# Kernel tuning notes

Hardware: AMD Instinct MI355X
Metric: run time of the kernel (lower is better)

Reference implementation:

```python
import jax, jax.numpy as jnp
import numpy as np

H_DIM = 1024
NHEADS = 16
HEAD = H_DIM // NHEADS


def setup_inputs() -> dict:
    key = jax.random.key(0)
    ks = jax.random.split(key, 7)
    B, T = 2, 2048
    s = 1.0 / np.sqrt(H_DIM)
    return {
        "x": jax.random.normal(ks[0], (B, T, H_DIM), dtype=jnp.float32),
        "Wq": jax.random.uniform(ks[1], (H_DIM, H_DIM), jnp.float32, -s, s),
        "bq": jax.random.uniform(ks[2], (H_DIM,), jnp.float32, -s, s),
        "Wk": jax.random.uniform(ks[3], (H_DIM, H_DIM), jnp.float32, -s, s),
        "bk": jax.random.uniform(ks[4], (H_DIM,), jnp.float32, -s, s),
        "Wv": jax.random.uniform(ks[5], (H_DIM, H_DIM), jnp.float32, -s, s),
        "bv": jax.random.uniform(ks[6], (H_DIM,), jnp.float32, -s, s),
    }


def _split_heads(a, B, T):
    # [B, T, h_dim] -> [B, nH, T, head]
    return a.reshape(B, T, NHEADS, HEAD).transpose(0, 2, 1, 3)


def reference(x, Wq, bq, Wk, bk, Wv, bv):
    B, T, allH = x.shape
    q = _split_heads(x @ Wq.T + bq, B, T)
    k = _split_heads(x @ Wk.T + bk, B, T)
    v = _split_heads(x @ Wv.T + bv, B, T)
    # NOTE: original scales by sqrt(h_dim) (full hidden), not sqrt(head_dim)
    att = jnp.einsum("bhqd,bhkd->bhqk", q, k) / jnp.sqrt(jnp.float32(allH))
    causal = jnp.tril(jnp.ones((T, T), dtype=bool))
    att = jnp.where(causal, att, -jnp.inf)
    att = jax.nn.softmax(att, axis=-1)
    out = jnp.einsum("bhqk,bhkd->bhqd", att, v)
    return out.transpose(0, 2, 1, 3).reshape(B, T, allH)
```

## Files before the change

### kernel.cpp

```cpp
#include <hip/hip_runtime.h>
#include <math.h>

typedef __bf16 bf16;
typedef __bf16 bf16x8 __attribute__((ext_vector_type(8)));
typedef __bf16 bf16x4 __attribute__((ext_vector_type(4)));
typedef __bf16 bf16x2 __attribute__((ext_vector_type(2)));
typedef float floatx4 __attribute__((ext_vector_type(4)));
typedef float floatx16 __attribute__((ext_vector_type(16)));
typedef unsigned int uintx4 __attribute__((ext_vector_type(4)));

#define T_SEQ 2048
#define NH 16
#define HD 64
#define HDIM 1024
#define BATCH 2
#define SCALE 0.03125f

static __device__ __forceinline__ floatx4 mfma16(bf16x8 a, bf16x8 b, floatx4 c) {
  return __builtin_amdgcn_mfma_f32_16x16x32_bf16(a, b, c, 0, 0, 0);
}
static __device__ __forceinline__ floatx16 mfma32(bf16x8 a, bf16x8 b, floatx16 c) {
  return __builtin_amdgcn_mfma_f32_32x32x16_bf16(a, b, c, 0, 0, 0);
}

static __device__ __forceinline__ unsigned int packbf(float a, float b) {
  bf16x2 t; t[0] = (bf16)a; t[1] = (bf16)b;
  return __builtin_bit_cast(unsigned int, t);
}

static __device__ __forceinline__ bf16x8 cvt_pack(floatx4 lo, floatx4 hi) {
  bf16x8 r;
  r[0] = (bf16)lo[0]; r[1] = (bf16)lo[1]; r[2] = (bf16)lo[2]; r[3] = (bf16)lo[3];
  r[4] = (bf16)hi[0]; r[5] = (bf16)hi[1]; r[6] = (bf16)hi[2]; r[7] = (bf16)hi[3];
  return r;
}

typedef const __attribute__((address_space(1))) void* gas_ptr;
typedef __attribute__((address_space(3))) void* las_ptr;
static __device__ __forceinline__ void load_lds16(const bf16* g, bf16* l) {
  __builtin_amdgcn_global_load_lds((gas_ptr)g, (las_ptr)l, 16, 0, 0);
}

__global__ __launch_bounds__(256) void cvt_f32_bf16(
    const float* __restrict__ x, const float* __restrict__ Wq,
    const float* __restrict__ Wk, const float* __restrict__ Wv,
    bf16* __restrict__ xb, bf16* __restrict__ wb) {
  const int seg = blockIdx.y;
  const float* src; bf16* dst; int n;
  if (seg == 0)      { src = x;  dst = xb;                 n = BATCH * T_SEQ * HDIM; }
  else if (seg == 1) { src = Wq; dst = wb;                 n = HDIM * HDIM; }
  else if (seg == 2) { src = Wk; dst = wb + HDIM * HDIM;   n = HDIM * HDIM; }
  else               { src = Wv; dst = wb + 2*HDIM*HDIM;   n = HDIM * HDIM; }
  const int i4 = (blockIdx.x * 256 + threadIdx.x) * 4;
  if (i4 < n) {
    floatx4 v = *(const floatx4*)(src + i4);
    bf16x4 o; o[0]=(bf16)v[0]; o[1]=(bf16)v[1]; o[2]=(bf16)v[2]; o[3]=(bf16)v[3];
    *(bf16x4*)(dst + i4) = o;
  }
}

__global__ __launch_bounds__(256) void qkv_gemm_lds(
    const bf16* __restrict__ xb, const bf16* __restrict__ wb,
    const float* __restrict__ bq, const float* __restrict__ bk,
    const float* __restrict__ bv, bf16* __restrict__ qkv) {
  __shared__ __align__(16) bf16 smem[16384];

  const int m0  = blockIdx.x * 128;
  const int n0g = blockIdx.y * 128;
  const int z   = n0g >> 10;
  const float* bias = (z == 0) ? bq : (z == 1) ? bk : bv;
  bf16* out = qkv + (size_t)z * BATCH * T_SEQ * HDIM;

  const int lane = threadIdx.x & 63;
  const int w    = threadIdx.x >> 6;
  const int l15  = lane & 15;
  const int quad = lane >> 4;
  const int wm = w & 1, wn = w >> 1;

  const int srow = w * 32 + (lane >> 2);
  const int scol = (lane & 3) * 8;
  const bf16* aG0 = xb + (size_t)(m0 + srow) * HDIM + scol;
  const bf16* aG1 = xb + (size_t)(m0 + srow + 16) * HDIM + scol;
  const bf16* bG0 = wb + (size_t)(n0g + srow) * HDIM + scol;
  const bf16* bG1 = wb + (size_t)(n0g + srow + 16) * HDIM + scol;

#define GSTAGE(BUF, KOFF)                                                    \
  {                                                                          \
    bf16* aB = smem + (BUF) * 4096;                                          \
    bf16* bB = smem + 8192 + (BUF) * 4096;                                   \
    load_lds16(aG0 + (KOFF), aB + (w * 32) * 32);                            \
    load_lds16(aG1 + (KOFF), aB + (w * 32 + 16) * 32);                       \
    load_lds16(bG0 + (KOFF), bB + (w * 32) * 32);                            \
    load_lds16(bG1 + (KOFF), bB + (w * 32 + 16) * 32);                       \
  }

  floatx4 acc[4][4] = {};

  GSTAGE(0, 0);
  __syncthreads();

  for (int k0 = 0; k0 < 32; ++k0) {
    const int cur = k0 & 1;
    if (k0 < 31) GSTAGE(cur ^ 1, (k0 + 1) * 32);

    const bf16* A = smem + cur * 4096;
    const bf16* B = smem + 8192 + cur * 4096;

    bf16x8 af[4], bf[4];
#pragma unroll
    for (int i = 0; i < 4; ++i)
      af[i] = *(const bf16x8*)(A + (wm * 64 + i * 16 + l15) * 32 + quad * 8);
#pragma unroll
    for (int jj = 0; jj < 4; ++jj)
      bf[jj] = *(const bf16x8*)(B + (wn * 64 + jj * 16 + l15) * 32 + quad * 8);
#pragma unroll
    for (int i = 0; i < 4; ++i)
#pragma unroll
      for (int jj = 0; jj < 4; ++jj)
        acc[i][jj] = mfma16(af[i], bf[jj], acc[i][jj]);

    __syncthreads();
  }
#undef GSTAGE

  const size_t bhS = (size_t)T_SEQ * HD;
  for (int jj = 0; jj < 4; ++jj) {
    const int nloc = (n0g + wn * 64 + jj * 16 + l15) & (HDIM - 1);
    const float bvv = bias[nloc];
    const int h = nloc >> 6, d = nloc & (HD - 1);
    for (int i = 0; i < 4; ++i) {
      for (int r = 0; r < 4; ++r) {
        const int gm = m0 + wm * 64 + i * 16 + quad * 4 + r;
        const int bb = gm >> 11, t = gm & (T_SEQ - 1);
        const bf16 val = (bf16)(acc[i][jj][r] + bvv);
        bf16* obh = out + (size_t)(bb * NH + h) * bhS;
        if (z == 0) {
          obh[(size_t)t * HD + d] = val;
        } else if (z == 1) {
          obh[(t >> 5) * 2048 + (d >> 4) * 512 +
              ((t & 31) + ((d >> 3) & 1) * 32) * 8 + (d & 7)] = val;
        } else {
          obh[(t >> 5) * 2048 + (((t >> 4) & 1) + ((d >> 5) << 1)) * 512 +
              ((d & 31) + ((t >> 3) & 1) * 32) * 8 + (t & 7)] = val;
        }
      }
    }
  }
}

#define LSTR 40

__global__ __launch_bounds__(256) void qkv_gemm_f32(
    const float* __restrict__ x,
    const float* __restrict__ Wq, const float* __restrict__ bq,
    const float* __restrict__ Wk, const float* __restrict__ bk,
    const float* __restrict__ Wv, const float* __restrict__ bv,
    bf16* __restrict__ qkv) {
  __shared__ __align__(16) bf16 As[128 * LSTR];
  __shared__ __align__(16) bf16 Bs[128 * LSTR];

  const int n0g = blockIdx.y * 128;
  const int z   = n0g >> 10;
  const int n0  = n0g & (HDIM - 1);
  const float* W    = (z == 0) ? Wq : (z == 1) ? Wk : Wv;
  const float* bias = (z == 0) ? bq : (z == 1) ? bk : bv;
  bf16* out = qkv + (size_t)z * BATCH * T_SEQ * HDIM;
  const int m0 = blockIdx.x * 128;

  const int lane = threadIdx.x & 63;
  const int w    = threadIdx.x >> 6;
  const int l15  = lane & 15;
  const int quad = lane >> 4;
  const int wm = w & 1, wn = w >> 1;

  const int srow  = threadIdx.x >> 1;
  const int shalf = threadIdx.x & 1;
  const float* aSrc = x + (size_t)(m0 + srow) * HDIM + shalf * 16;
  const float* bSrc = W + (size_t)(n0 + srow) * HDIM + shalf * 16;
  bf16* aDst = As + srow * LSTR + shalf * 16;
  bf16* bDst = Bs + srow * LSTR + shalf * 16;

  floatx4 acc[4][4] = {};

  for (int k0 = 0; k0 < HDIM; k0 += 32) {
    floatx4 a0 = *(const floatx4*)(aSrc + k0);
    floatx4 a1 = *(const floatx4*)(aSrc + k0 + 4);
    floatx4 a2 = *(const floatx4*)(aSrc + k0 + 8);
    floatx4 a3 = *(const floatx4*)(aSrc + k0 + 12);
    floatx4 b0 = *(const floatx4*)(bSrc + k0);
    floatx4 b1 = *(const floatx4*)(bSrc + k0 + 4);
    floatx4 b2 = *(const floatx4*)(bSrc + k0 + 8);
    floatx4 b3 = *(const floatx4*)(bSrc + k0 + 12);

    __syncthreads();
    *(bf16x8*)(aDst)     = cvt_pack(a0, a1);
    *(bf16x8*)(aDst + 8) = cvt_pack(a2, a3);
    *(bf16x8*)(bDst)     = cvt_pack(b0, b1);
    *(bf16x8*)(bDst + 8) = cvt_pack(b2, b3);
    __syncthreads();

    bf16x8 af[4], bff[4];
    for (int i = 0; i < 4; ++i)
      af[i] = *(const bf16x8*)(As + (wm * 64 + i * 16 + l15) * LSTR + quad * 8);
    for (int jj = 0; jj < 4; ++jj)
      bff[jj] = *(const bf16x8*)(Bs + (wn * 64 + jj * 16 + l15) * LSTR + quad * 8);
    for (int i = 0; i < 4; ++i)
      for (int jj = 0; jj < 4; ++jj)
        acc[i][jj] = mfma16(af[i], bff[jj], acc[i][jj]);
  }

  for (int jj = 0; jj < 4; ++jj) {
    const int nloc = n0 + wn * 64 + jj * 16 + l15;
    const float bvv = bias[nloc];
    const int h = nloc >> 6, d = nloc & (HD - 1);
    for (int i = 0; i < 4; ++i) {
      for (int r = 0; r < 4; ++r) {
        const int gm = m0 + wm * 64 + i * 16 + quad * 4 + r;
        const int bb = gm >> 11, t = gm & (T_SEQ - 1);
        out[((size_t)((bb * NH + h) * T_SEQ) + t) * HD + d] = (bf16)(acc[i][jj][r] + bvv);
      }
    }
  }
}

#define ASTEP(G, QF, O0, O1, LL, DIAG)                                         \
  {                                                                            \
    const bf16* kp_ = Kb + (G) * 2048 + lane * 8;                              \
    bf16x8 kf0 = *(const bf16x8*)(kp_);                                        \
    bf16x8 kf1 = *(const bf16x8*)(kp_ + 512);                                  \
    bf16x8 kf2 = *(const bf16x8*)(kp_ + 1024);                                 \
    bf16x8 kf3 = *(const bf16x8*)(kp_ + 1536);                                 \
    const bf16* vp_ = Vb + (G) * 2048 + lane * 8;                              \
    bf16x8 v00 = *(const bf16x8*)(vp_);                                        \
    bf16x8 v01 = *(const bf16x8*)(vp_ + 512);                                  \
    bf16x8 v10 = *(const bf16x8*)(vp_ + 1024);                                 \
    bf16x8 v11 = *(const bf16x8*)(vp_ + 1536);                                 \
    floatx16 s = {};                                                           \
    s = mfma32(kf0, QF[0], s);                                                 \
    s = mfma32(kf1, QF[1], s);                                                 \
    s = mfma32(kf2, QF[2], s);                                                 \
    s = mfma32(kf3, QF[3], s);                                                 \
    float pp[16];                                                              \
    _Pragma("unroll")                                                          \
    for (int r = 0; r < 16; ++r) pp[r] = __expf(s[r]);                         \
    if (DIAG) {                                                                \
      _Pragma("unroll")                                                        \
      for (int r = 0; r < 16; ++r) {                                           \
        const int krow = (r & 3) + 8 * (r >> 2) + 4 * hf;                      \
        if (krow > l31) pp[r] = 0.f;                                           \
      }                                                                        \
    }                                                                          \
    float psum = 0.f;                                                          \
    _Pragma("unroll")                                                          \
    for (int r = 0; r < 16; ++r) psum += pp[r];                                \
    LL += psum;                                                                \
    unsigned int Dg[4][2], Xg[4][2];                                           \
    _Pragma("unroll")                                                          \
    for (int a = 0; a < 4; ++a) {                                              \
      Dg[a][0] = packbf(pp[4 * a + 0], pp[4 * a + 1]);                         \
      Dg[a][1] = packbf(pp[4 * a + 2], pp[4 * a + 3]);                         \
    }                                                                          \
    _Pragma("unroll")                                                          \
    for (int a = 0; a < 4; ++a) {                                              \
      Xg[a][0] = (unsigned int)__shfl_xor((int)Dg[a][0], 32, 64);              \
      Xg[a][1] = (unsigned int)__shfl_xor((int)Dg[a][1], 32, 64);              \
    }                                                                          \
    uintx4 f0u, f1u;                                                           \
    f0u[0] = hf ? Xg[1][0] : Dg[0][0];                                         \
    f0u[1] = hf ? Xg[1][1] : Dg[0][1];                                         \
    f0u[2] = hf ? Dg[1][0] : Xg[0][0];                                         \
    f0u[3] = hf ? Dg[1][1] : Xg[0][1];                                         \
    f1u[0] = hf ? Xg[3][0] : Dg[2][0];                                         \
    f1u[1] = hf ? Xg[3][1] : Dg[2][1];                                         \
    f1u[2] = hf ? Dg[3][0] : Xg[2][0];                                         \
    f1u[3] = hf ? Dg[3][1] : Xg[2][1];                                         \
    bf16x8 pf0 = __builtin_bit_cast(bf16x8, f0u);                              \
    bf16x8 pf1 = __builtin_bit_cast(bf16x8, f1u);                              \
    O0 = mfma32(v00, pf0, O0);                                                 \
    O0 = mfma32(v01, pf1, O0);                                                 \
    O1 = mfma32(v10, pf0, O1);                                                 \
    O1 = mfma32(v11, pf1, O1);                                                 \
  }

__global__ __launch_bounds__(256, 4) void attn_v13(
    const bf16* __restrict__ qkv, float* __restrict__ out) {
  const bf16* Q = qkv;

  __shared__ float ps[4][64][33];

  const int lane = threadIdx.x & 63;
  const int w    = threadIdx.x >> 6;
  const int l31  = lane & 31;
  const int hf   = lane >> 5;

  const int lin = blockIdx.x + (blockIdx.y << 5);
  const int bh  = ((lin & 7) << 2) + ((lin >> 3) & 3);
  const int pi  = lin >> 5;

  const int qtA = pi, qtB = 63 - pi;
  const int q0A = qtA * 32, q0B = qtB * 32;
  const int SA = qtA + 1;

  const bf16* Qb = Q + (size_t)bh * T_SEQ * HD;
  const bf16* Kb = qkv + (size_t)BATCH * T_SEQ * HDIM + (size_t)bh * T_SEQ * HD;
  const bf16* Vb = qkv + (size_t)2 * BATCH * T_SEQ * HDIM + (size_t)bh * T_SEQ * HD;
  const int b = bh >> 4, hh = bh & (NH - 1);

  bf16x8 qfA[4];
#pragma unroll
  for (int kk = 0; kk < 4; ++kk) {
    qfA[kk] = *(const bf16x8*)(Qb + (size_t)(q0A + l31) * HD + kk * 16 + hf * 8);
#pragma unroll
    for (int e = 0; e < 8; ++e) qfA[kk][e] = (bf16)((float)qfA[kk][e] * SCALE);
  }

  floatx16 oA0 = {}, oA1 = {};
  float laccA = 0.f;

  int g = w;
  for (; g < SA; g += 4)
    ASTEP(g, qfA, oA0, oA1, laccA, g == SA - 1);

  laccA += __shfl_xor(laccA, 32, 64);

#pragma unroll
  for (int r = 0; r < 16; ++r) {
    ps[w][lane][r]      = oA0[r];
    ps[w][lane][16 + r] = oA1[r];
  }
  ps[w][lane][32] = laccA;
  __syncthreads();
  {
    const float ls = ps[0][lane][32] + ps[1][lane][32] +
                     ps[2][lane][32] + ps[3][lane][32];
    const float inv = 1.f / ls;
    float* obA = out + ((size_t)(b * T_SEQ + q0A + l31)) * HDIM + hh * HD;
#pragma unroll
    for (int i = 0; i < 8; ++i) {
      const int rr = 8 * w + i;
      const float sv = ps[0][lane][rr] + ps[1][lane][rr] +
                       ps[2][lane][rr] + ps[3][lane][rr];
      const int r = rr & 15;
      const int drow = (r & 3) + 8 * (r >> 2) + 4 * hf + ((rr >= 16) ? 32 : 0);
      obA[drow] = sv * inv;
    }
  }
  __syncthreads();

  bf16x8 qfB[4];
#pragma unroll
  for (int kk = 0; kk < 4; ++kk) {
    qfB[kk] = *(const bf16x8*)(Qb + (size_t)(q0B + l31) * HD + kk * 16 + hf * 8);
#pragma unroll
    for (int e = 0; e < 8; ++e) qfB[kk][e] = (bf16)((float)qfB[kk][e] * SCALE);
  }

  floatx16 oB0 = {}, oB1 = {};
  float laccB = 0.f;

  for (; g < 65; g += 4)
    ASTEP(g - SA, qfB, oB0, oB1, laccB, g == 64);

  laccB += __shfl_xor(laccB, 32, 64);

#pragma unroll
  for (int r = 0; r < 16; ++r) {
    ps[w][lane][r]      = oB0[r];
    ps[w][lane][16 + r] = oB1[r];
  }
  ps[w][lane][32] = laccB;
  __syncthreads();
  {
    const float ls = ps[0][lane][32] + ps[1][lane][32] +
                     ps[2][lane][32] + ps[3][lane][32];
    const float inv = 1.f / ls;
    float* obB = out + ((size_t)(b * T_SEQ + q0B + l31)) * HDIM + hh * HD;
#pragma unroll
    for (int i = 0; i < 8; ++i) {
      const int rr = 8 * w + i;
      const float sv = ps[0][lane][rr] + ps[1][lane][rr] +
                       ps[2][lane][rr] + ps[3][lane][rr];
      const int r = rr & 15;
      const int drow = (r & 3) + 8 * (r >> 2) + 4 * hf + ((rr >= 16) ? 32 : 0);
      obB[drow] = sv * inv;
    }
  }
}

#define PSTR 40

__global__ __launch_bounds__(256) void attn_v4(
    const bf16* __restrict__ qkv, float* __restrict__ out) {
  const bf16* Q = qkv;
  const bf16* K = qkv + (size_t)BATCH * T_SEQ * HDIM;
  const bf16* V = K + (size_t)BATCH * T_SEQ * HDIM;

  __shared__ __align__(16) bf16 pl[4 * 16 * PSTR];

  const int lane = threadIdx.x & 63;
  const int w    = threadIdx.x >> 6;
  const int l15  = lane & 15;
  const int quad = lane >> 4;

  const int bh = blockIdx.x;
  const int j  = blockIdx.y;
  const bf16* Qb = Q + (size_t)bh * T_SEQ * HD;
  const bf16* Kb = K + (size_t)bh * T_SEQ * HD;
  const bf16* Vb = V + (size_t)bh * T_SEQ * HD;
  const int b = bh >> 4, h = bh & (NH - 1);

  const int qt = (w == 0) ? j : (w == 1) ? (63 - j) : (w == 2) ? (64 + j) : (127 - j);
  const int q0 = qt * 16;

  bf16* pw = pl + w * 16 * PSTR;

  bf16x8 qf0 = *(const bf16x8*)(Qb + (size_t)(q0 + l15) * HD + quad * 8);
  bf16x8 qf1 = *(const bf16x8*)(Qb + (size_t)(q0 + l15) * HD + 32 + quad * 8);
  for (int e = 0; e < 8; ++e) {
    qf0[e] = (bf16)((float)qf0[e] * SCALE);
    qf1[e] = (bf16)((float)qf1[e] * SCALE);
  }

  floatx4 o[4] = {};
  float lacc[4] = {0.f, 0.f, 0.f, 0.f};

  const int S = (qt >> 1) + 1;

  for (int s0 = 0; s0 < S; ++s0) {
    const int kv = s0 * 32;

    bf16 ve[4][8];
    for (int jjj = 0; jjj < 8; ++jjj) {
      const bf16* vrow = Vb + (size_t)(kv + quad * 8 + jjj) * HD + l15;
      for (int dt = 0; dt < 4; ++dt) ve[dt][jjj] = vrow[dt * 16];
    }

    floatx4 sa[2];
    for (int nt = 0; nt < 2; ++nt) {
      const int kbase = kv + nt * 16;
      bf16x8 k0 = *(const bf16x8*)(Kb + (size_t)(kbase + l15) * HD + quad * 8);
      bf16x8 k1 = *(const bf16x8*)(Kb + (size_t)(kbase + l15) * HD + 32 + quad * 8);
      floatx4 s = {};
      s = mfma16(qf0, k0, s);
      s = mfma16(qf1, k1, s);
      sa[nt] = s;
    }

    float p[2][4];
    for (int nt = 0; nt < 2; ++nt)
      for (int r = 0; r < 4; ++r) p[nt][r] = __expf(sa[nt][r]);
    if (s0 == S - 1) {
      for (int nt = 0; nt < 2; ++nt) {
        const int kg = kv + nt * 16 + l15;
        for (int r = 0; r < 4; ++r) {
          const int qg = q0 + quad * 4 + r;
          if (kg > qg) p[nt][r] = 0.f;
        }
      }
    }
    for (int r = 0; r < 4; ++r) lacc[r] += p[0][r] + p[1][r];

    for (int nt = 0; nt < 2; ++nt)
      for (int r = 0; r < 4; ++r)
        pw[(quad * 4 + r) * PSTR + nt * 16 + l15] = (bf16)p[nt][r];
    __asm__ __volatile__("s_waitcnt lgkmcnt(0)" ::: "memory");
    const bf16x8 pf = *(const bf16x8*)(pw + l15 * PSTR + quad * 8);

    for (int dt = 0; dt < 4; ++dt) {
      bf16x8 vf;
      for (int jjj = 0; jjj < 8; ++jjj) vf[jjj] = ve[dt][jjj];
      o[dt] = mfma16(pf, vf, o[dt]);
    }
  }

  for (int r = 0; r < 4; ++r) {
    float v = lacc[r];
    for (int off = 1; off < 16; off <<= 1) v += __shfl_xor(v, off, 64);
    lacc[r] = v;
  }

  for (int dt = 0; dt < 4; ++dt) {
    for (int r = 0; r < 4; ++r) {
      const int t = q0 + quad * 4 + r;
      out[((size_t)(b * T_SEQ + t) * HDIM) + h * HD + dt * 16 + l15] =
          o[dt][r] / lacc[r];
    }
  }
}

extern "C" void kernel_launch(void* const* d_in, const int* in_sizes, int n_in,
                              void* d_out, int out_size, void* d_ws, size_t ws_size,
                              hipStream_t stream) {
  const float* x  = (const float*)d_in[0];
  const float* Wq = (const float*)d_in[1];
  const float* bq = (const float*)d_in[2];
  const float* Wk = (const float*)d_in[3];
  const float* bk = (const float*)d_in[4];
  const float* Wv = (const float*)d_in[5];
  const float* bv = (const float*)d_in[6];
  float* out = (float*)d_out;

  const size_t elems = (size_t)BATCH * T_SEQ * HDIM;
  bf16* qkv  = (bf16*)d_ws;
  bf16* xbuf = qkv + 3 * elems;
  bf16* wbuf = xbuf + elems;

  const bool fast = ws_size >= (size_t)39 * 1024 * 1024;
  dim3 g1(BATCH * T_SEQ / 128, 3 * HDIM / 128);
  if (fast) {
    cvt_f32_bf16<<<dim3(4096, 4), 256, 0, stream>>>(x, Wq, Wk, Wv, xbuf, wbuf);
    qkv_gemm_lds<<<g1, 256, 0, stream>>>(xbuf, wbuf, bq, bk, bv, qkv);
    attn_v13<<<dim3(BATCH * NH, 32), 256, 0, stream>>>(qkv, out);
  } else {
    qkv_gemm_f32<<<g1, 256, 0, stream>>>(x, Wq, bq, Wk, bk, Wv, bv, qkv);
    attn_v4<<<dim3(BATCH * NH, 32), 256, 0, stream>>>(qkv, out);
  }
}
```

Measured before the change: 151.5 us.

## Process two query tiles per K/V load in attention kernel

```diff
diff --git a/kernel.cpp b/kernel.cpp
--- a/kernel.cpp
+++ b/kernel.cpp
@@ -223,18 +223,8 @@
   }
 }
 
-#define ASTEP(G, QF, O0, O1, LL, DIAG)                                         \
+#define TBODY(QF, DIAG, O0, O1, LL)                                            \
   {                                                                            \
-    const bf16* kp_ = Kb + (G) * 2048 + lane * 8;                              \
-    bf16x8 kf0 = *(const bf16x8*)(kp_);                                        \
-    bf16x8 kf1 = *(const bf16x8*)(kp_ + 512);                                  \
-    bf16x8 kf2 = *(const bf16x8*)(kp_ + 1024);                                 \
-    bf16x8 kf3 = *(const bf16x8*)(kp_ + 1536);                                 \
-    const bf16* vp_ = Vb + (G) * 2048 + lane * 8;                              \
-    bf16x8 v00 = *(const bf16x8*)(vp_);                                        \
-    bf16x8 v01 = *(const bf16x8*)(vp_ + 512);                                  \
-    bf16x8 v10 = *(const bf16x8*)(vp_ + 1024);                                 \
-    bf16x8 v11 = *(const bf16x8*)(vp_ + 1536);                                 \
     floatx16 s = {};                                                           \
     s = mfma32(kf0, QF[0], s);                                                 \
     s = mfma32(kf1, QF[1], s);                                                 \
@@ -282,10 +272,49 @@
     O1 = mfma32(v11, pf1, O1);                                                 \
   }
 
-__global__ __launch_bounds__(256, 4) void attn_v13(
+#define ASTEP2(G, T0, QF0a, QF1a)                                              \
+  {                                                                            \
+    const int g_ = (G);                                                        \
+    const bf16* kp_ = Kb + g_ * 2048 + lane * 8;                               \
+    bf16x8 kf0 = *(const bf16x8*)(kp_);                                        \
+    bf16x8 kf1 = *(const bf16x8*)(kp_ + 512);                                  \
+    bf16x8 kf2 = *(const bf16x8*)(kp_ + 1024);                                 \
+    bf16x8 kf3 = *(const bf16x8*)(kp_ + 1536);                                 \
+    const bf16* vp_ = Vb + g_ * 2048 + lane * 8;                               \
+    bf16x8 v00 = *(const bf16x8*)(vp_);                                        \
+    bf16x8 v01 = *(const bf16x8*)(vp_ + 512);                                  \
+    bf16x8 v10 = *(const bf16x8*)(vp_ + 1024);                                 \
+    bf16x8 v11 = *(const bf16x8*)(vp_ + 1536);                                 \
+    if (g_ <= (T0)) TBODY(QF0a, g_ == (T0), o00, o01, l0);                     \
+    TBODY(QF1a, g_ == (T0) + 1, o10, o11, l1);                                 \
+  }
+
+#define COMBINE(O0, O1, LL, QROW)                                              \
+  {                                                                            \
+    _Pragma("unroll")                                                          \
+    for (int r = 0; r < 16; ++r) {                                             \
+      ps[w][lane][r]      = O0[r];                                             \
+      ps[w][lane][16 + r] = O1[r];                                             \
+    }                                                                          \
+    ps[w][lane][32] = LL;                                                      \
+    __syncthreads();                                                           \
+    const float ls = ps[0][lane][32] + ps[1][lane][32] +                       \
+                     ps[2][lane][32] + ps[3][lane][32];                        \
+    const float inv = 1.f / ls;                                                \
+    float* ob = out + ((size_t)(b * T_SEQ + (QROW))) * HDIM + hh * HD;         \
+    _Pragma("unroll")                                                          \
+    for (int i = 0; i < 8; ++i) {                                              \
+      const int rr = 8 * w + i;                                                \
+      const float sv = ps[0][lane][rr] + ps[1][lane][rr] +                     \
+                       ps[2][lane][rr] + ps[3][lane][rr];                      \
+      const int r = rr & 15;                                                   \
+      const int drow = (r & 3) + 8 * (r >> 2) + 4 * hf + ((rr >= 16) ? 32 : 0);\
+      ob[drow] = sv * inv;                                                     \
+    }                                                                          \
+  }
+
+__global__ __launch_bounds__(256, 2) void attn_v14(
     const bf16* __restrict__ qkv, float* __restrict__ out) {
-  const bf16* Q = qkv;
-
   __shared__ float ps[4][64][33];
 
   const int lane = threadIdx.x & 63;
@@ -295,96 +324,70 @@
 
   const int lin = blockIdx.x + (blockIdx.y << 5);
   const int bh  = ((lin & 7) << 2) + ((lin >> 3) & 3);
-  const int pi  = lin >> 5;
-
-  const int qtA = pi, qtB = 63 - pi;
-  const int q0A = qtA * 32, q0B = qtB * 32;
-  const int SA = qtA + 1;
-
-  const bf16* Qb = Q + (size_t)bh * T_SEQ * HD;
+  const int p   = lin >> 5;
+
+  const int a0 = 2 * p;
+  const int b0 = 62 - 2 * p;
+  const int NA = 2 * p + 2;
+
+  const bf16* Qb = qkv + (size_t)bh * T_SEQ * HD;
   const bf16* Kb = qkv + (size_t)BATCH * T_SEQ * HDIM + (size_t)bh * T_SEQ * HD;
   const bf16* Vb = qkv + (size_t)2 * BATCH * T_SEQ * HDIM + (size_t)bh * T_SEQ * HD;
   const int b = bh >> 4, hh = bh & (NH - 1);
 
-  bf16x8 qfA[4];
+  bf16x8 qf0[4], qf1[4];
+  floatx16 o00, o01, o10, o11;
+  float l0, l1;
+  int m = w;
+
 #pragma unroll
   for (int kk = 0; kk < 4; ++kk) {
-    qfA[kk] = *(const bf16x8*)(Qb + (size_t)(q0A + l31) * HD + kk * 16 + hf * 8);
-#pragma unroll
-    for (int e = 0; e < 8; ++e) qfA[kk][e] = (bf16)((float)qfA[kk][e] * SCALE);
-  }
-
-  floatx16 oA0 = {}, oA1 = {};
-  float laccA = 0.f;
-
-  int g = w;
-  for (; g < SA; g += 4)
-    ASTEP(g, qfA, oA0, oA1, laccA, g == SA - 1);
-
-  laccA += __shfl_xor(laccA, 32, 64);
-
-#pragma unroll
-  for (int r = 0; r < 16; ++r) {
-    ps[w][lane][r]      = oA0[r];
-    ps[w][lane][16 + r] = oA1[r];
-  }
-  ps[w][lane][32] = laccA;
+    qf0[kk] = *(const bf16x8*)(Qb + (size_t)(a0 * 32 + l31) * HD + kk * 16 + hf * 8);
+    qf1[kk] = *(const bf16x8*)(Qb + (size_t)(a0 * 32 + 32 + l31) * HD + kk * 16 + hf * 8);
+#pragma unroll
+    for (int e = 0; e < 8; ++e) {
+      qf0[kk][e] = (bf16)((float)qf0[kk][e] * SCALE);
+      qf1[kk][e] = (bf16)((float)qf1[kk][e] * SCALE);
+    }
+  }
+  o00 = (floatx16){}; o01 = (floatx16){};
+  o10 = (floatx16){}; o11 = (floatx16){};
+  l0 = 0.f; l1 = 0.f;
+
+  for (; m < NA; m += 4)
+    ASTEP2(m, a0, qf0, qf1);
+
+  l0 += __shfl_xor(l0, 32, 64);
+  l1 += __shfl_xor(l1, 32, 64);
+
+  COMBINE(o00, o01, l0, a0 * 32 + l31);
   __syncthreads();
-  {
-    const float ls = ps[0][lane][32] + ps[1][lane][32] +
-                     ps[2][lane][32] + ps[3][lane][32];
-    const float inv = 1.f / ls;
-    float* obA = out + ((size_t)(b * T_SEQ + q0A + l31)) * HDIM + hh * HD;
-#pragma unroll
-    for (int i = 0; i < 8; ++i) {
-      const int rr = 8 * w + i;
-      const float sv = ps[0][lane][rr] + ps[1][lane][rr] +
-                       ps[2][lane][rr] + ps[3][lane][rr];
-      const int r = rr & 15;
-      const int drow = (r & 3) + 8 * (r >> 2) + 4 * hf + ((rr >= 16) ? 32 : 0);
-      obA[drow] = sv * inv;
-    }
-  }
+  COMBINE(o10, o11, l1, a0 * 32 + 32 + l31);
   __syncthreads();
 
-  bf16x8 qfB[4];
 #pragma unroll
   for (int kk = 0; kk < 4; ++kk) {
-    qfB[kk] = *(const bf16x8*)(Qb + (size_t)(q0B + l31) * HD + kk * 16 + hf * 8);
-#pragma unroll
-    for (int e = 0; e < 8; ++e) qfB[kk][e] = (bf16)((float)qfB[kk][e] * SCALE);
-  }
-
-  floatx16 oB0 = {}, oB1 = {};
-  float laccB = 0.f;
-
-  for (; g < 65; g += 4)
-    ASTEP(g - SA, qfB, oB0, oB1, laccB, g == 64);
-
-  laccB += __shfl_xor(laccB, 32, 64);
-
-#pragma unroll
-  for (int r = 0; r < 16; ++r) {
-    ps[w][lane][r]      = oB0[r];
-    ps[w][lane][16 + r] = oB1[r];
-  }
-  ps[w][lane][32] = laccB;
+    qf0[kk] = *(const bf16x8*)(Qb + (size_t)(b0 * 32 + l31) * HD + kk * 16 + hf * 8);
+    qf1[kk] = *(const bf16x8*)(Qb + (size_t)(b0 * 32 + 32 + l31) * HD + kk * 16 + hf * 8);
+#pragma unroll
+    for (int e = 0; e < 8; ++e) {
+      qf0[kk][e] = (bf16)((float)qf0[kk][e] * SCALE);
+      qf1[kk][e] = (bf16)((float)qf1[kk][e] * SCALE);
+    }
+  }
+  o00 = (floatx16){}; o01 = (floatx16){};
+  o10 = (floatx16){}; o11 = (floatx16){};
+  l0 = 0.f; l1 = 0.f;
+
+  for (; m < 66; m += 4)
+    ASTEP2(m - NA, b0, qf0, qf1);
+
+  l0 += __shfl_xor(l0, 32, 64);
+  l1 += __shfl_xor(l1, 32, 64);
+
+  COMBINE(o00, o01, l0, b0 * 32 + l31);
   __syncthreads();
-  {
-    const float ls = ps[0][lane][32] + ps[1][lane][32] +
-                     ps[2][lane][32] + ps[3][lane][32];
-    const float inv = 1.f / ls;
-    float* obB = out + ((size_t)(b * T_SEQ + q0B + l31)) * HDIM + hh * HD;
-#pragma unroll
-    for (int i = 0; i < 8; ++i) {
-      const int rr = 8 * w + i;
-      const float sv = ps[0][lane][rr] + ps[1][lane][rr] +
-                       ps[2][lane][rr] + ps[3][lane][rr];
-      const int r = rr & 15;
-      const int drow = (r & 3) + 8 * (r >> 2) + 4 * hf + ((rr >= 16) ? 32 : 0);
-      obB[drow] = sv * inv;
-    }
-  }
+  COMBINE(o10, o11, l1, b0 * 32 + 32 + l31);
 }
 
 #define PSTR 40
@@ -510,7 +513,7 @@
   if (fast) {
     cvt_f32_bf16<<<dim3(4096, 4), 256, 0, stream>>>(x, Wq, Wk, Wv, xbuf, wbuf);
     qkv_gemm_lds<<<g1, 256, 0, stream>>>(xbuf, wbuf, bq, bk, bv, qkv);
-    attn_v13<<<dim3(BATCH * NH, 32), 256, 0, stream>>>(qkv, out);
+    attn_v14<<<dim3(32, 16), 256, 0, stream>>>(qkv, out);
   } else {
     qkv_gemm_f32<<<g1, 256, 0, stream>>>(x, Wq, bq, Wk, bk, Wv, bv, qkv);
     attn_v4<<<dim3(BATCH * NH, 32), 256, 0, stream>>>(qkv, out);
```

Result: no change. 151.9 us (+0.2%).
